# Performance work log

Measured on AMD Instinct MI355X. Metric: run time of the kernel, lower is better.

## Reference

```python
import jax, jax.numpy as jnp
import numpy as np

UNITS = 512
INPUT_SIZE = 512
BATCH = 64
SEQ_LEN = 512


def setup_inputs() -> dict:
    key = jax.random.key(0)
    k_x, k_wx, k_wh = jax.random.split(key, 3)
    scale_x = 1.0 / np.sqrt(INPUT_SIZE)
    scale_h = 1.0 / np.sqrt(UNITS)
    return {
        "x": jax.random.normal(k_x, (BATCH, SEQ_LEN, INPUT_SIZE), dtype=jnp.float32),
        "h0": jnp.zeros((BATCH, UNITS), dtype=jnp.float32),
        "c0": jnp.zeros((BATCH, UNITS), dtype=jnp.float32),
        "Wx": jax.random.normal(k_wx, (INPUT_SIZE, 4 * UNITS), dtype=jnp.float32) * scale_x,
        "Wh": jax.random.normal(k_wh, (UNITS, 4 * UNITS), dtype=jnp.float32) * scale_h,
        "b": jnp.zeros((4 * UNITS,), dtype=jnp.float32),
    }


def reference(x, h0, c0, Wx, Wh, b):
    """LSTM layer over full sequence; returns stacked hidden states [seq_len, batch, units]
    (matching TensorArray.stack() time-major output of the original)."""

    def step(carry, xt):
        h, c = carry
        # fused gate pre-activations: [batch, 4*units]
        z = xt @ Wx + h @ Wh + b
        i, f, g, o = jnp.split(z, 4, axis=-1)  # Keras gate order: i, f, c(g), o
        i = jax.nn.sigmoid(i)
        f = jax.nn.sigmoid(f)
        g = jnp.tanh(g)
        o = jax.nn.sigmoid(o)
        c_new = f * c + i * g
        h_new = o * jnp.tanh(c_new)
        return (h_new, c_new), h_new

    xs = jnp.swapaxes(x, 0, 1)  # [seq_len, batch, input_size]
    (_, _), hs = jax.lax.scan(step, (h0, c0), xs)
    return hs  # [seq_len, batch, units]
```

## Files before the change

kernel.cpp:

```cpp
#include <hip/hip_runtime.h>
#include <stdint.h>


#define OFF_XBF   0ull
#define OFF_HU    33562624ull

typedef short short8 __attribute__((ext_vector_type(8)));
typedef float f32x4 __attribute__((ext_vector_type(4)));
typedef unsigned u32x4 __attribute__((ext_vector_type(4)));

__device__ __forceinline__ unsigned f32_to_bf16(float f) {
    union { float f; unsigned u; } v; v.f = f;
    unsigned u = v.u;
    unsigned r = u + 0x7FFFu + ((u >> 16) & 1u);
    return r >> 16;
}

__global__ void prep_kernel(const float* __restrict__ x,
                            const float* __restrict__ h0,
                            unsigned char* __restrict__ ws) {
    long long i = (long long)blockIdx.x * blockDim.x + threadIdx.x;
    if (i < 2097152) {
        const float4* xs = (const float4*)x + i * 2;
        float4 a = xs[0], b = xs[1];
        unsigned w0 = f32_to_bf16(a.x) | (f32_to_bf16(a.y) << 16);
        unsigned w1 = f32_to_bf16(a.z) | (f32_to_bf16(a.w) << 16);
        unsigned w2 = f32_to_bf16(b.x) | (f32_to_bf16(b.y) << 16);
        unsigned w3 = f32_to_bf16(b.z) | (f32_to_bf16(b.w) << 16);
        uint4 o; o.x = w0; o.y = w1; o.z = w2; o.w = w3;
        ((uint4*)(ws + OFF_XBF))[i] = o;
        return;
    }
    i -= 2097152;
    if (i < 16384) {
        int b = (int)(i >> 8), p = (int)(i & 255);
        unsigned lo = f32_to_bf16(h0[b * 512 + 2 * p]);
        unsigned hi = f32_to_bf16(h0[b * 512 + 2 * p + 1]);
        ((unsigned long long*)(ws + OFF_HU))[(long long)b * 256 + p] =
            (unsigned long long)(lo | (hi << 16)) | (1ull << 32);
    }
}

#define SPIN_LOAD(BASEPTR, TAGV, H0V, H1V)                                     \
    {                                                                          \
        u32x4 p0, p1, p2, p3;                                                  \
        for (;;) {                                                             \
            asm volatile(                                                      \
                "global_load_dwordx4 %0, %4, off sc0 sc1\n\t"                  \
                "global_load_dwordx4 %1, %4, off offset:16 sc0 sc1\n\t"        \
                "global_load_dwordx4 %2, %4, off offset:32 sc0 sc1\n\t"        \
                "global_load_dwordx4 %3, %4, off offset:48 sc0 sc1\n\t"        \
                "s_waitcnt vmcnt(0)"                                           \
                : "=v"(p0), "=v"(p1), "=v"(p2), "=v"(p3)                       \
                : "v"(BASEPTR)                                                 \
                : "memory");                                                   \
            unsigned bad = (p0.y ^ (TAGV)) | (p0.w ^ (TAGV))                   \
                         | (p1.y ^ (TAGV)) | (p1.w ^ (TAGV))                   \
                         | (p2.y ^ (TAGV)) | (p2.w ^ (TAGV))                   \
                         | (p3.y ^ (TAGV)) | (p3.w ^ (TAGV));                  \
            if (!bad) {                                                        \
                H0V.x = p0.x; H0V.y = p0.z; H0V.z = p1.x; H0V.w = p1.z;        \
                H1V.x = p2.x; H1V.y = p2.z; H1V.z = p3.x; H1V.w = p3.z;        \
                break;                                                         \
            }                                                                  \
            __builtin_amdgcn_s_sleep(0);                                       \
        }                                                                      \
    }

__launch_bounds__(256, 1)
__global__ void lstm_kernel(const float* __restrict__ c0,
                            const float* __restrict__ bias,
                            const float* __restrict__ Wx,
                            const float* __restrict__ Wh,
                            float* __restrict__ out,
                            unsigned char* __restrict__ ws) {
    const int tid  = threadIdx.x;
    const int bid  = blockIdx.x;
    const int s    = bid & 7;
    const int jg   = bid >> 3;
    const int lane = tid & 63;
    const int wave = tid >> 6;
    const int nl   = lane & 15;
    const int q    = lane >> 4;
    const int up   = nl & 3;
    const int g    = nl >> 2;

    const unsigned short* xbf = (const unsigned short*)(ws + OFF_XBF);
    unsigned long long* Hu = (unsigned long long*)(ws + OFF_HU);

    __shared__ __align__(16) unsigned char lds[20736];
    float* lds_out = (float*)(lds + 16640);

    const int ncol = g * 512 + jg * 16 + wave * 4 + up;
    short8 fWh[16], fWx[16];
#pragma unroll
    for (int kt = 0; kt < 16; ++kt) {
        const int k0 = kt * 32 + q * 8;
        short8 vh, vx;
#pragma unroll
        for (int j = 0; j < 8; ++j) {
            vh[j] = (short)f32_to_bf16(Wh[(long long)(k0 + j) * 2048 + ncol]);
            vx[j] = (short)f32_to_bf16(Wx[(long long)(k0 + j) * 2048 + ncol]);
        }
        fWh[kt] = vh; fWx[kt] = vx;
    }

    const int ub = jg * 16 + wave * 4 + up;
    const float bi  = bias[ub];
    const float bf_ = bias[512 + ub];
    const float bg  = bias[1024 + ub];
    const float bo  = bias[1536 + ub];

    float cr[4];
#pragma unroll
    for (int r = 0; r < 4; ++r) {
        const int m = q * 4 + r;
        cr[r] = (q < 2) ? c0[(8 * s + m) * 512 + ub] : 0.f;
    }

    const int sm = tid >> 5, sc = tid & 31;
    const int sb = 8 * s + sm;
    const unsigned* xsrc_base = (const unsigned*)xbf + (long long)sb * 131072 + sc * 8;
    unsigned long long* hsrc_base = Hu + sb * 256 + sc * 8;
    uint4* xdst = (uint4*)(lds + sm * 1040 + sc * 32);
    uint4* hdst = (uint4*)(lds + 8320 + sm * 1040 + sc * 32);

    const unsigned char* axp = lds + nl * 1040 + q * 16;
    const unsigned char* ahp = lds + 8320 + nl * 1040 + q * 16;
    const short8 zfrag = {0, 0, 0, 0, 0, 0, 0, 0};

    const int gbase = (lane & 0x30) | (lane & 3);
    const int sl0 = gbase, sl1 = gbase | 4, sl2 = gbase | 8, sl3 = gbase | 12;

    uint4 px0 = *(const uint4*)(xsrc_base);
    uint4 px1 = *(const uint4*)(xsrc_base + 4);
    xdst[0] = px0; xdst[1] = px1;
    px0 = *(const uint4*)(xsrc_base + 256);
    px1 = *(const uint4*)(xsrc_base + 256 + 4);
    __syncthreads();

    f32x4 accx;
    {
        f32x4 a0 = {0.f,0.f,0.f,0.f}, a1 = {0.f,0.f,0.f,0.f};
#pragma unroll
        for (int kt = 0; kt < 16; kt += 2) {
            short8 v0 = (nl < 8) ? *(const short8*)(axp + kt * 64) : zfrag;
            short8 v1 = (nl < 8) ? *(const short8*)(axp + kt * 64 + 64) : zfrag;
            a0 = __builtin_amdgcn_mfma_f32_16x16x32_bf16(v0, fWx[kt], a0, 0, 0, 0);
            a1 = __builtin_amdgcn_mfma_f32_16x16x32_bf16(v1, fWx[kt + 1], a1, 0, 0, 0);
        }
        accx = a0 + a1;
    }
    {
        const unsigned char* hs0 = (const unsigned char*)hsrc_base;
        uint4 h0v, h1v;
        SPIN_LOAD(hs0, 1u, h0v, h1v);
        hdst[0] = h0v; hdst[1] = h1v;
    }
    __syncthreads();

    for (int t = 0; t < 512; ++t) {
        const int wb = (t + 1) & 1;

        f32x4 acch;
        {
            f32x4 a0 = {0.f,0.f,0.f,0.f}, a1 = {0.f,0.f,0.f,0.f};
#pragma unroll
            for (int kt = 0; kt < 16; kt += 2) {
                short8 v0 = (nl < 8) ? *(const short8*)(ahp + kt * 64) : zfrag;
                short8 v1 = (nl < 8) ? *(const short8*)(ahp + kt * 64 + 64) : zfrag;
                a0 = __builtin_amdgcn_mfma_f32_16x16x32_bf16(v0, fWh[kt], a0, 0, 0, 0);
                a1 = __builtin_amdgcn_mfma_f32_16x16x32_bf16(v1, fWh[kt + 1], a1, 0, 0, 0);
            }
            acch = a0 + a1;
        }

        float hn[4]; unsigned hb[4];
#pragma unroll
        for (int r = 0; r < 4; ++r) {
            float zs = accx[r] + acch[r];
            float z0 = __shfl(zs, sl0, 64) + bi;
            float z1 = __shfl(zs, sl1, 64) + bf_;
            float z2 = __shfl(zs, sl2, 64) + bg;
            float z3 = __shfl(zs, sl3, 64) + bo;
            float ig = __fdividef(1.f, 1.f + __expf(-z0));
            float fg = __fdividef(1.f, 1.f + __expf(-z1));
            float z2c = fminf(fmaxf(z2, -20.f), 20.f);
            float e2 = __expf(2.f * z2c);
            float gg = __fdividef(e2 - 1.f, e2 + 1.f);
            float og = __fdividef(1.f, 1.f + __expf(-z3));
            float cn = fg * cr[r] + ig * gg;
            cr[r] = cn;
            float cnc = fminf(fmaxf(cn, -20.f), 20.f);
            float ec = __expf(2.f * cnc);
            hn[r] = og * __fdividef(ec - 1.f, ec + 1.f);
            hb[r] = f32_to_bf16(hn[r]);
        }
        unsigned oth[4];
#pragma unroll
        for (int r = 0; r < 4; ++r)
            oth[r] = (unsigned)__shfl((int)hb[r], lane ^ 1, 64);

        if (q < 2 && g == 0) {
#pragma unroll
            for (int r = 0; r < 4; ++r)
                lds_out[(t & 7) * 128 + (q * 4 + r) * 16 + wave * 4 + up] = hn[r];
            if ((up & 1) == 0) {
#pragma unroll
                for (int r = 0; r < 4; ++r) {
                    unsigned long long v = (unsigned long long)(hb[r] | (oth[r] << 16))
                                         | ((unsigned long long)(unsigned)(t + 2) << 32);
                    __hip_atomic_store(Hu + (size_t)wb * 16384 + (8 * s + q * 4 + r) * 256
                                           + jg * 8 + wave * 2 + (up >> 1),
                                       v, __ATOMIC_RELAXED, __HIP_MEMORY_SCOPE_AGENT);
                }
            }
        }

        xdst[0] = px0; xdst[1] = px1;
        {
            const int tp = (t + 2 < 512) ? (t + 2) : 511;
            px0 = *(const uint4*)(xsrc_base + tp * 256);
            px1 = *(const uint4*)(xsrc_base + tp * 256 + 4);
        }
        __syncthreads();

        if ((t & 7) == 7) {
            const int stp = tid >> 5, brow = (tid >> 2) & 7, qd = tid & 3;
            float4 v = *(const float4*)(lds_out + stp * 128 + brow * 16 + qd * 4);
            *(float4*)(out + (long long)(t - 7 + stp) * 32768
                           + (8 * s + brow) * 512 + jg * 16 + qd * 4) = v;
        }

        {
            f32x4 a0 = {0.f,0.f,0.f,0.f}, a1 = {0.f,0.f,0.f,0.f};
#pragma unroll
            for (int kt = 0; kt < 16; kt += 2) {
                short8 v0 = (nl < 8) ? *(const short8*)(axp + kt * 64) : zfrag;
                short8 v1 = (nl < 8) ? *(const short8*)(axp + kt * 64 + 64) : zfrag;
                a0 = __builtin_amdgcn_mfma_f32_16x16x32_bf16(v0, fWx[kt], a0, 0, 0, 0);
                a1 = __builtin_amdgcn_mfma_f32_16x16x32_bf16(v1, fWx[kt + 1], a1, 0, 0, 0);
            }
            accx = a0 + a1;
        }

        {
            const unsigned char* hs = (const unsigned char*)hsrc_base
                                    + (size_t)wb * 131072;
            const unsigned tag = (unsigned)(t + 2);
            uint4 h0v, h1v;
            SPIN_LOAD(hs, tag, h0v, h1v);
            hdst[0] = h0v; hdst[1] = h1v;
        }
        __syncthreads();
    }
}

extern "C" void kernel_launch(void* const* d_in, const int* in_sizes, int n_in,
                              void* d_out, int out_size, void* d_ws, size_t ws_size,
                              hipStream_t stream) {
    const float* x  = (const float*)d_in[0];
    const float* h0 = (const float*)d_in[1];
    const float* c0 = (const float*)d_in[2];
    const float* Wx = (const float*)d_in[3];
    const float* Wh = (const float*)d_in[4];
    const float* b  = (const float*)d_in[5];
    unsigned char* ws = (unsigned char*)d_ws;
    float* out = (float*)d_out;

    const long long n0 = 2097152 + 16384;
    const int blocks0 = (int)((n0 + 255) / 256);
    hipLaunchKernelGGL(prep_kernel, dim3(blocks0), dim3(256), 0, stream, x, h0, ws);
    hipLaunchKernelGGL(lstm_kernel, dim3(256), dim3(256), 0, stream,
                       c0, b, Wx, Wh, out, ws);
}
```

Measured before the change: 1.746 ms.

## Gate hidden-state spin loads on compact per-group ready flags

```diff
diff --git a/kernel.cpp b/kernel.cpp
--- a/kernel.cpp
+++ b/kernel.cpp
@@ -3,6 +3,7 @@
 
 
 #define OFF_XBF   0ull
+#define OFF_FLAG  33554432ull
 #define OFF_HU    33562624ull
 
 typedef short short8 __attribute__((ext_vector_type(8)));
@@ -38,8 +39,27 @@
         unsigned hi = f32_to_bf16(h0[b * 512 + 2 * p + 1]);
         ((unsigned long long*)(ws + OFF_HU))[(long long)b * 256 + p] =
             (unsigned long long)(lo | (hi << 16)) | (1ull << 32);
+        return;
+    }
+    i -= 16384;
+    if (i < 1024) {
+        ((unsigned*)(ws + OFF_FLAG))[i] = (i < 512) ? 0x00010001u : 0u;
     }
 }
+
+#define FLAG_GATE(FBASE, TAGV)                                                 \
+    {                                                                          \
+        const unsigned expect_ = (TAGV) * 0x10001u;                            \
+        const unsigned* fp_ = (FBASE) + lane;                                  \
+        for (;;) {                                                             \
+            unsigned fv_;                                                      \
+            asm volatile("global_load_dword %0, %1, off sc0 sc1\n\t"           \
+                         "s_waitcnt vmcnt(0)"                                  \
+                         : "=v"(fv_) : "v"(fp_) : "memory");                   \
+            if (!__any((int)(fv_ ^ expect_))) break;                           \
+            __builtin_amdgcn_s_sleep(0);                                       \
+        }                                                                      \
+    }
 
 #define SPIN_LOAD(BASEPTR, TAGV, H0V, H1V)                                     \
     {                                                                          \
@@ -152,6 +172,8 @@
         accx = a0 + a1;
     }
     {
+        const unsigned* fb = (const unsigned*)(ws + OFF_FLAG) + (size_t)s * 64;
+        FLAG_GATE(fb, 1u);
         const unsigned char* hs0 = (const unsigned char*)hsrc_base;
         uint4 h0v, h1v;
         SPIN_LOAD(hs0, 1u, h0v, h1v);
@@ -218,6 +240,16 @@
         }
 
         xdst[0] = px0; xdst[1] = px1;
+
+        asm volatile("s_waitcnt vmcnt(0)" ::: "memory");
+        if (lane == 0) {
+            unsigned short* fp = (unsigned short*)(ws + OFF_FLAG)
+                               + (size_t)(wb * 8 + s) * 128 + jg * 4 + wave;
+            unsigned tv = (unsigned)(t + 2);
+            asm volatile("global_store_short %0, %1, off sc0 sc1"
+                         :: "v"(fp), "v"(tv) : "memory");
+        }
+
         {
             const int tp = (t + 2 < 512) ? (t + 2) : 511;
             px0 = *(const uint4*)(xsrc_base + tp * 256);
@@ -245,9 +277,12 @@
         }
 
         {
+            const unsigned* fb = (const unsigned*)(ws + OFF_FLAG)
+                               + (size_t)(wb * 8 + s) * 64;
+            const unsigned tag = (unsigned)(t + 2);
+            FLAG_GATE(fb, tag);
             const unsigned char* hs = (const unsigned char*)hsrc_base
                                     + (size_t)wb * 131072;
-            const unsigned tag = (unsigned)(t + 2);
             uint4 h0v, h1v;
             SPIN_LOAD(hs, tag, h0v, h1v);
             hdst[0] = h0v; hdst[1] = h1v;
@@ -268,7 +303,7 @@
     unsigned char* ws = (unsigned char*)d_ws;
     float* out = (float*)d_out;
 
-    const long long n0 = 2097152 + 16384;
+    const long long n0 = 2097152 + 16384 + 1024;
     const int blocks0 = (int)((n0 + 255) / 256);
     hipLaunchKernelGGL(prep_kernel, dim3(blocks0), dim3(256), 0, stream, x, h0, ws);
     hipLaunchKernelGGL(lstm_kernel, dim3(256), dim3(256), 0, stream,
```

Result: slower. 2.271 ms (+30.1%).

## Publish hidden state to dual buffers with local and system-scope polling

Applied to the files above, without the earlier changes.

```diff
diff --git a/kernel.cpp b/kernel.cpp
--- a/kernel.cpp
+++ b/kernel.cpp
@@ -3,7 +3,8 @@
 
 
 #define OFF_XBF   0ull
-#define OFF_HU    33562624ull
+#define OFF_HL    33554432ull
+#define OFF_HG    33816576ull
 
 typedef short short8 __attribute__((ext_vector_type(8)));
 typedef float f32x4 __attribute__((ext_vector_type(4)));
@@ -36,33 +37,47 @@
         int b = (int)(i >> 8), p = (int)(i & 255);
         unsigned lo = f32_to_bf16(h0[b * 512 + 2 * p]);
         unsigned hi = f32_to_bf16(h0[b * 512 + 2 * p + 1]);
-        ((unsigned long long*)(ws + OFF_HU))[(long long)b * 256 + p] =
+        unsigned long long v =
             (unsigned long long)(lo | (hi << 16)) | (1ull << 32);
-    }
-}
-
-#define SPIN_LOAD(BASEPTR, TAGV, H0V, H1V)                                     \
+        ((unsigned long long*)(ws + OFF_HL))[(long long)b * 256 + p] = v;
+        ((unsigned long long*)(ws + OFF_HG))[(long long)b * 256 + p] = v;
+    }
+}
+
+#define POLL_ONCE(BASEPTR, CPOL, TAGV, OKV, H0V, H1V)                          \
     {                                                                          \
         u32x4 p0, p1, p2, p3;                                                  \
+        asm volatile(                                                          \
+            "global_load_dwordx4 %0, %4, off " CPOL "\n\t"                     \
+            "global_load_dwordx4 %1, %4, off offset:16 " CPOL "\n\t"           \
+            "global_load_dwordx4 %2, %4, off offset:32 " CPOL "\n\t"           \
+            "global_load_dwordx4 %3, %4, off offset:48 " CPOL "\n\t"           \
+            "s_waitcnt vmcnt(0)"                                               \
+            : "=v"(p0), "=v"(p1), "=v"(p2), "=v"(p3)                           \
+            : "v"(BASEPTR)                                                     \
+            : "memory");                                                       \
+        unsigned bad = (p0.y ^ (TAGV)) | (p0.w ^ (TAGV))                       \
+                     | (p1.y ^ (TAGV)) | (p1.w ^ (TAGV))                       \
+                     | (p2.y ^ (TAGV)) | (p2.w ^ (TAGV))                       \
+                     | (p3.y ^ (TAGV)) | (p3.w ^ (TAGV));                      \
+        OKV = (bad == 0u);                                                     \
+        if (OKV) {                                                             \
+            H0V.x = p0.x; H0V.y = p0.z; H0V.z = p1.x; H0V.w = p1.z;            \
+            H1V.x = p2.x; H1V.y = p2.z; H1V.z = p3.x; H1V.w = p3.z;            \
+        }                                                                      \
+    }
+
+#define SPIN_DUAL(LPTR, GPTR, TAGV, H0V, H1V)                                  \
+    {                                                                          \
+        int ok_ = 0, it_ = 0;                                                  \
         for (;;) {                                                             \
-            asm volatile(                                                      \
-                "global_load_dwordx4 %0, %4, off sc0 sc1\n\t"                  \
-                "global_load_dwordx4 %1, %4, off offset:16 sc0 sc1\n\t"        \
-                "global_load_dwordx4 %2, %4, off offset:32 sc0 sc1\n\t"        \
-                "global_load_dwordx4 %3, %4, off offset:48 sc0 sc1\n\t"        \
-                "s_waitcnt vmcnt(0)"                                           \
-                : "=v"(p0), "=v"(p1), "=v"(p2), "=v"(p3)                       \
-                : "v"(BASEPTR)                                                 \
-                : "memory");                                                   \
-            unsigned bad = (p0.y ^ (TAGV)) | (p0.w ^ (TAGV))                   \
-                         | (p1.y ^ (TAGV)) | (p1.w ^ (TAGV))                   \
-                         | (p2.y ^ (TAGV)) | (p2.w ^ (TAGV))                   \
-                         | (p3.y ^ (TAGV)) | (p3.w ^ (TAGV));                  \
-            if (!bad) {                                                        \
-                H0V.x = p0.x; H0V.y = p0.z; H0V.z = p1.x; H0V.w = p1.z;        \
-                H1V.x = p2.x; H1V.y = p2.z; H1V.z = p3.x; H1V.w = p3.z;        \
-                break;                                                         \
+            POLL_ONCE(LPTR, "sc0", TAGV, ok_, H0V, H1V);                       \
+            if (ok_) break;                                                    \
+            if ((it_ & 7) == 7) {                                              \
+                POLL_ONCE(GPTR, "sc0 sc1", TAGV, ok_, H0V, H1V);               \
+                if (ok_) break;                                                \
             }                                                                  \
+            ++it_;                                                             \
             __builtin_amdgcn_s_sleep(0);                                       \
         }                                                                      \
     }
@@ -86,7 +101,8 @@
     const int g    = nl >> 2;
 
     const unsigned short* xbf = (const unsigned short*)(ws + OFF_XBF);
-    unsigned long long* Hu = (unsigned long long*)(ws + OFF_HU);
+    unsigned long long* HuL = (unsigned long long*)(ws + OFF_HL);
+    unsigned long long* HuG = (unsigned long long*)(ws + OFF_HG);
 
     __shared__ __align__(16) unsigned char lds[20736];
     float* lds_out = (float*)(lds + 16640);
@@ -121,7 +137,8 @@
     const int sm = tid >> 5, sc = tid & 31;
     const int sb = 8 * s + sm;
     const unsigned* xsrc_base = (const unsigned*)xbf + (long long)sb * 131072 + sc * 8;
-    unsigned long long* hsrc_base = Hu + sb * 256 + sc * 8;
+    const unsigned char* hl_base = (const unsigned char*)(HuL + sb * 256 + sc * 8);
+    const unsigned char* hg_base = (const unsigned char*)(HuG + sb * 256 + sc * 8);
     uint4* xdst = (uint4*)(lds + sm * 1040 + sc * 32);
     uint4* hdst = (uint4*)(lds + 8320 + sm * 1040 + sc * 32);
 
@@ -152,9 +169,8 @@
         accx = a0 + a1;
     }
     {
-        const unsigned char* hs0 = (const unsigned char*)hsrc_base;
         uint4 h0v, h1v;
-        SPIN_LOAD(hs0, 1u, h0v, h1v);
+        SPIN_DUAL(hl_base, hg_base, 1u, h0v, h1v);
         hdst[0] = h0v; hdst[1] = h1v;
     }
     __syncthreads();
@@ -210,9 +226,13 @@
                 for (int r = 0; r < 4; ++r) {
                     unsigned long long v = (unsigned long long)(hb[r] | (oth[r] << 16))
                                          | ((unsigned long long)(unsigned)(t + 2) << 32);
-                    __hip_atomic_store(Hu + (size_t)wb * 16384 + (8 * s + q * 4 + r) * 256
-                                           + jg * 8 + wave * 2 + (up >> 1),
-                                       v, __ATOMIC_RELAXED, __HIP_MEMORY_SCOPE_AGENT);
+                    const size_t idx = (size_t)wb * 16384
+                                     + (size_t)(8 * s + q * 4 + r) * 256
+                                     + jg * 8 + wave * 2 + (up >> 1);
+                    asm volatile("global_store_dwordx2 %0, %1, off sc0"
+                                 :: "v"(HuL + idx), "v"(v) : "memory");
+                    asm volatile("global_store_dwordx2 %0, %1, off sc0 sc1"
+                                 :: "v"(HuG + idx), "v"(v) : "memory");
                 }
             }
         }
@@ -245,11 +265,11 @@
         }
 
         {
-            const unsigned char* hs = (const unsigned char*)hsrc_base
-                                    + (size_t)wb * 131072;
+            const unsigned char* hl = hl_base + (size_t)wb * 131072;
+            const unsigned char* hg = hg_base + (size_t)wb * 131072;
             const unsigned tag = (unsigned)(t + 2);
             uint4 h0v, h1v;
-            SPIN_LOAD(hs, tag, h0v, h1v);
+            SPIN_DUAL(hl, hg, tag, h0v, h1v);
             hdst[0] = h0v; hdst[1] = h1v;
         }
         __syncthreads();
```

Result: slower. 2.133 ms (+22.2%).

## Process two batch slices per block, halving grid to 128 blocks

Applied to the files above, without the earlier changes.

```diff
diff --git a/kernel.cpp b/kernel.cpp
--- a/kernel.cpp
+++ b/kernel.cpp
@@ -67,6 +67,73 @@
         }                                                                      \
     }
 
+#define MFMA_LOOP(AP, W, ACC)                                                  \
+    {                                                                          \
+        f32x4 a0_ = {0.f,0.f,0.f,0.f}, a1_ = {0.f,0.f,0.f,0.f};                \
+        _Pragma("unroll")                                                      \
+        for (int kt = 0; kt < 16; kt += 2) {                                   \
+            short8 v0_ = (nl < 8) ? *(const short8*)((AP) + kt * 64) : zfrag;  \
+            short8 v1_ = (nl < 8) ? *(const short8*)((AP) + kt * 64 + 64) : zfrag; \
+            a0_ = __builtin_amdgcn_mfma_f32_16x16x32_bf16(v0_, (W)[kt], a0_, 0, 0, 0); \
+            a1_ = __builtin_amdgcn_mfma_f32_16x16x32_bf16(v1_, (W)[kt + 1], a1_, 0, 0, 0); \
+        }                                                                      \
+        ACC = a0_ + a1_;                                                       \
+    }
+
+#define GATES_PUBLISH(ACCX, ACCH, CR, LDSOUT, SS)                              \
+    {                                                                          \
+        float hn[4]; unsigned hb[4];                                           \
+        _Pragma("unroll")                                                      \
+        for (int r = 0; r < 4; ++r) {                                          \
+            float zs = (ACCX)[r] + (ACCH)[r];                                  \
+            float z0 = __shfl(zs, sl0, 64) + bi;                               \
+            float z1 = __shfl(zs, sl1, 64) + bf_;                              \
+            float z2 = __shfl(zs, sl2, 64) + bg;                               \
+            float z3 = __shfl(zs, sl3, 64) + bo;                               \
+            float ig = __fdividef(1.f, 1.f + __expf(-z0));                     \
+            float fg = __fdividef(1.f, 1.f + __expf(-z1));                     \
+            float z2c = fminf(fmaxf(z2, -20.f), 20.f);                         \
+            float e2 = __expf(2.f * z2c);                                      \
+            float gg = __fdividef(e2 - 1.f, e2 + 1.f);                         \
+            float og = __fdividef(1.f, 1.f + __expf(-z3));                     \
+            float cn = fg * (CR)[r] + ig * gg;                                 \
+            (CR)[r] = cn;                                                      \
+            float cnc = fminf(fmaxf(cn, -20.f), 20.f);                         \
+            float ec = __expf(2.f * cnc);                                      \
+            hn[r] = og * __fdividef(ec - 1.f, ec + 1.f);                       \
+            hb[r] = f32_to_bf16(hn[r]);                                        \
+        }                                                                      \
+        unsigned oth[4];                                                       \
+        _Pragma("unroll")                                                      \
+        for (int r = 0; r < 4; ++r)                                            \
+            oth[r] = (unsigned)__shfl((int)hb[r], lane ^ 1, 64);               \
+        if (q < 2 && g == 0) {                                                 \
+            _Pragma("unroll")                                                  \
+            for (int r = 0; r < 4; ++r)                                        \
+                (LDSOUT)[(t & 7) * 128 + (q * 4 + r) * 16 + wave * 4 + up] = hn[r]; \
+            if ((up & 1) == 0) {                                               \
+                _Pragma("unroll")                                              \
+                for (int r = 0; r < 4; ++r) {                                  \
+                    unsigned long long v = (unsigned long long)(hb[r] | (oth[r] << 16)) \
+                                         | ((unsigned long long)(unsigned)(t + 2) << 32); \
+                    unsigned long long* pp = Hu + (size_t)wb * 16384           \
+                                           + (size_t)(8 * (SS) + q * 4 + r) * 256 \
+                                           + jg * 8 + wave * 2 + (up >> 1);    \
+                    asm volatile("global_store_dwordx2 %0, %1, off sc0 sc1"    \
+                                 :: "v"(pp), "v"(v) : "memory");               \
+                }                                                              \
+            }                                                                  \
+        }                                                                      \
+    }
+
+#define OUT_BURST(LDSOUT, SS)                                                  \
+    {                                                                          \
+        const int stp = tid >> 5, brow = (tid >> 2) & 7, qd = tid & 3;         \
+        float4 v = *(const float4*)((LDSOUT) + stp * 128 + brow * 16 + qd * 4); \
+        *(float4*)(out + (long long)(t - 7 + stp) * 32768                      \
+                       + (8 * (SS) + brow) * 512 + jg * 16 + qd * 4) = v;      \
+    }
+
 __launch_bounds__(256, 1)
 __global__ void lstm_kernel(const float* __restrict__ c0,
                             const float* __restrict__ bias,
@@ -75,9 +142,10 @@
                             float* __restrict__ out,
                             unsigned char* __restrict__ ws) {
     const int tid  = threadIdx.x;
-    const int bid  = blockIdx.x;
-    const int s    = bid & 7;
-    const int jg   = bid >> 3;
+    const int p    = blockIdx.x >> 5;
+    const int jg   = blockIdx.x & 31;
+    const int sA   = p;
+    const int sB   = p + 4;
     const int lane = tid & 63;
     const int wave = tid >> 6;
     const int nl   = lane & 15;
@@ -88,8 +156,9 @@
     const unsigned short* xbf = (const unsigned short*)(ws + OFF_XBF);
     unsigned long long* Hu = (unsigned long long*)(ws + OFF_HU);
 
-    __shared__ __align__(16) unsigned char lds[20736];
-    float* lds_out = (float*)(lds + 16640);
+    __shared__ __align__(16) unsigned char lds[41472];
+    float* lds_outA = (float*)(lds + 33280);
+    float* lds_outB = (float*)(lds + 37376);
 
     const int ncol = g * 512 + jg * 16 + wave * 4 + up;
     short8 fWh[16], fWx[16];
@@ -111,146 +180,108 @@
     const float bg  = bias[1024 + ub];
     const float bo  = bias[1536 + ub];
 
-    float cr[4];
+    float crA[4], crB[4];
 #pragma unroll
     for (int r = 0; r < 4; ++r) {
         const int m = q * 4 + r;
-        cr[r] = (q < 2) ? c0[(8 * s + m) * 512 + ub] : 0.f;
+        crA[r] = (q < 2) ? c0[(8 * sA + m) * 512 + ub] : 0.f;
+        crB[r] = (q < 2) ? c0[(8 * sB + m) * 512 + ub] : 0.f;
     }
 
     const int sm = tid >> 5, sc = tid & 31;
-    const int sb = 8 * s + sm;
-    const unsigned* xsrc_base = (const unsigned*)xbf + (long long)sb * 131072 + sc * 8;
-    unsigned long long* hsrc_base = Hu + sb * 256 + sc * 8;
-    uint4* xdst = (uint4*)(lds + sm * 1040 + sc * 32);
-    uint4* hdst = (uint4*)(lds + 8320 + sm * 1040 + sc * 32);
-
-    const unsigned char* axp = lds + nl * 1040 + q * 16;
-    const unsigned char* ahp = lds + 8320 + nl * 1040 + q * 16;
+    const int sbA = 8 * sA + sm, sbB = 8 * sB + sm;
+    const unsigned* xsrcA = (const unsigned*)xbf + (long long)sbA * 131072 + sc * 8;
+    const unsigned* xsrcB = (const unsigned*)xbf + (long long)sbB * 131072 + sc * 8;
+    unsigned long long* hsrcA = Hu + sbA * 256 + sc * 8;
+    unsigned long long* hsrcB = Hu + sbB * 256 + sc * 8;
+    uint4* xdstA = (uint4*)(lds + sm * 1040 + sc * 32);
+    uint4* xdstB = (uint4*)(lds + 8320 + sm * 1040 + sc * 32);
+    uint4* hdstA = (uint4*)(lds + 16640 + sm * 1040 + sc * 32);
+    uint4* hdstB = (uint4*)(lds + 24960 + sm * 1040 + sc * 32);
+
+    const unsigned char* axpA = lds + nl * 1040 + q * 16;
+    const unsigned char* axpB = lds + 8320 + nl * 1040 + q * 16;
+    const unsigned char* ahpA = lds + 16640 + nl * 1040 + q * 16;
+    const unsigned char* ahpB = lds + 24960 + nl * 1040 + q * 16;
     const short8 zfrag = {0, 0, 0, 0, 0, 0, 0, 0};
 
     const int gbase = (lane & 0x30) | (lane & 3);
     const int sl0 = gbase, sl1 = gbase | 4, sl2 = gbase | 8, sl3 = gbase | 12;
 
-    uint4 px0 = *(const uint4*)(xsrc_base);
-    uint4 px1 = *(const uint4*)(xsrc_base + 4);
-    xdst[0] = px0; xdst[1] = px1;
-    px0 = *(const uint4*)(xsrc_base + 256);
-    px1 = *(const uint4*)(xsrc_base + 256 + 4);
+    uint4 pA0 = *(const uint4*)(xsrcA);
+    uint4 pA1 = *(const uint4*)(xsrcA + 4);
+    uint4 pB0 = *(const uint4*)(xsrcB);
+    uint4 pB1 = *(const uint4*)(xsrcB + 4);
+    xdstA[0] = pA0; xdstA[1] = pA1;
+    xdstB[0] = pB0; xdstB[1] = pB1;
+    pA0 = *(const uint4*)(xsrcA + 256); pA1 = *(const uint4*)(xsrcA + 260);
+    pB0 = *(const uint4*)(xsrcB + 256); pB1 = *(const uint4*)(xsrcB + 260);
     __syncthreads();
 
-    f32x4 accx;
+    f32x4 accxA, accxB;
+    MFMA_LOOP(axpA, fWx, accxA);
+    MFMA_LOOP(axpB, fWx, accxB);
     {
-        f32x4 a0 = {0.f,0.f,0.f,0.f}, a1 = {0.f,0.f,0.f,0.f};
-#pragma unroll
-        for (int kt = 0; kt < 16; kt += 2) {
-            short8 v0 = (nl < 8) ? *(const short8*)(axp + kt * 64) : zfrag;
-            short8 v1 = (nl < 8) ? *(const short8*)(axp + kt * 64 + 64) : zfrag;
-            a0 = __builtin_amdgcn_mfma_f32_16x16x32_bf16(v0, fWx[kt], a0, 0, 0, 0);
-            a1 = __builtin_amdgcn_mfma_f32_16x16x32_bf16(v1, fWx[kt + 1], a1, 0, 0, 0);
-        }
-        accx = a0 + a1;
+        uint4 h0v, h1v;
+        SPIN_LOAD((const unsigned char*)hsrcA, 1u, h0v, h1v);
+        hdstA[0] = h0v; hdstA[1] = h1v;
     }
     {
-        const unsigned char* hs0 = (const unsigned char*)hsrc_base;
         uint4 h0v, h1v;
-        SPIN_LOAD(hs0, 1u, h0v, h1v);
-        hdst[0] = h0v; hdst[1] = h1v;
+        SPIN_LOAD((const unsigned char*)hsrcB, 1u, h0v, h1v);
+        hdstB[0] = h0v; hdstB[1] = h1v;
     }
     __syncthreads();
 
     for (int t = 0; t < 512; ++t) {
         const int wb = (t + 1) & 1;
 
-        f32x4 acch;
-        {
-            f32x4 a0 = {0.f,0.f,0.f,0.f}, a1 = {0.f,0.f,0.f,0.f};
-#pragma unroll
-            for (int kt = 0; kt < 16; kt += 2) {
-                short8 v0 = (nl < 8) ? *(const short8*)(ahp + kt * 64) : zfrag;
-                short8 v1 = (nl < 8) ? *(const short8*)(ahp + kt * 64 + 64) : zfrag;
-                a0 = __builtin_amdgcn_mfma_f32_16x16x32_bf16(v0, fWh[kt], a0, 0, 0, 0);
-                a1 = __builtin_amdgcn_mfma_f32_16x16x32_bf16(v1, fWh[kt + 1], a1, 0, 0, 0);
-            }
-            acch = a0 + a1;
-        }
-
-        float hn[4]; unsigned hb[4];
-#pragma unroll
-        for (int r = 0; r < 4; ++r) {
-            float zs = accx[r] + acch[r];
-            float z0 = __shfl(zs, sl0, 64) + bi;
-            float z1 = __shfl(zs, sl1, 64) + bf_;
-            float z2 = __shfl(zs, sl2, 64) + bg;
-            float z3 = __shfl(zs, sl3, 64) + bo;
-            float ig = __fdividef(1.f, 1.f + __expf(-z0));
-            float fg = __fdividef(1.f, 1.f + __expf(-z1));
-            float z2c = fminf(fmaxf(z2, -20.f), 20.f);
-            float e2 = __expf(2.f * z2c);
-            float gg = __fdividef(e2 - 1.f, e2 + 1.f);
-            float og = __fdividef(1.f, 1.f + __expf(-z3));
-            float cn = fg * cr[r] + ig * gg;
-            cr[r] = cn;
-            float cnc = fminf(fmaxf(cn, -20.f), 20.f);
-            float ec = __expf(2.f * cnc);
-            hn[r] = og * __fdividef(ec - 1.f, ec + 1.f);
-            hb[r] = f32_to_bf16(hn[r]);
-        }
-        unsigned oth[4];
-#pragma unroll
-        for (int r = 0; r < 4; ++r)
-            oth[r] = (unsigned)__shfl((int)hb[r], lane ^ 1, 64);
-
-        if (q < 2 && g == 0) {
-#pragma unroll
-            for (int r = 0; r < 4; ++r)
-                lds_out[(t & 7) * 128 + (q * 4 + r) * 16 + wave * 4 + up] = hn[r];
-            if ((up & 1) == 0) {
-#pragma unroll
-                for (int r = 0; r < 4; ++r) {
-                    unsigned long long v = (unsigned long long)(hb[r] | (oth[r] << 16))
-                                         | ((unsigned long long)(unsigned)(t + 2) << 32);
-                    __hip_atomic_store(Hu + (size_t)wb * 16384 + (8 * s + q * 4 + r) * 256
-                                           + jg * 8 + wave * 2 + (up >> 1),
-                                       v, __ATOMIC_RELAXED, __HIP_MEMORY_SCOPE_AGENT);
-                }
-            }
-        }
-
-        xdst[0] = px0; xdst[1] = px1;
+        {
+            f32x4 acch;
+            MFMA_LOOP(ahpA, fWh, acch);
+            GATES_PUBLISH(accxA, acch, crA, lds_outA, sA);
+        }
+
+        {
+            f32x4 acch;
+            MFMA_LOOP(ahpB, fWh, acch);
+            GATES_PUBLISH(accxB, acch, crB, lds_outB, sB);
+        }
+
+        xdstA[0] = pA0; xdstA[1] = pA1;
+        xdstB[0] = pB0; xdstB[1] = pB1;
         {
             const int tp = (t + 2 < 512) ? (t + 2) : 511;
-            px0 = *(const uint4*)(xsrc_base + tp * 256);
-            px1 = *(const uint4*)(xsrc_base + tp * 256 + 4);
+            pA0 = *(const uint4*)(xsrcA + tp * 256);
+            pA1 = *(const uint4*)(xsrcA + tp * 256 + 4);
+            pB0 = *(const uint4*)(xsrcB + tp * 256);
+            pB1 = *(const uint4*)(xsrcB + tp * 256 + 4);
         }
         __syncthreads();
 
         if ((t & 7) == 7) {
-            const int stp = tid >> 5, brow = (tid >> 2) & 7, qd = tid & 3;
-            float4 v = *(const float4*)(lds_out + stp * 128 + brow * 16 + qd * 4);
-            *(float4*)(out + (long long)(t - 7 + stp) * 32768
-                           + (8 * s + brow) * 512 + jg * 16 + qd * 4) = v;
-        }
-
-        {
-            f32x4 a0 = {0.f,0.f,0.f,0.f}, a1 = {0.f,0.f,0.f,0.f};
-#pragma unroll
-            for (int kt = 0; kt < 16; kt += 2) {
-                short8 v0 = (nl < 8) ? *(const short8*)(axp + kt * 64) : zfrag;
-                short8 v1 = (nl < 8) ? *(const short8*)(axp + kt * 64 + 64) : zfrag;
-                a0 = __builtin_amdgcn_mfma_f32_16x16x32_bf16(v0, fWx[kt], a0, 0, 0, 0);
-                a1 = __builtin_amdgcn_mfma_f32_16x16x32_bf16(v1, fWx[kt + 1], a1, 0, 0, 0);
-            }
-            accx = a0 + a1;
-        }
-
-        {
-            const unsigned char* hs = (const unsigned char*)hsrc_base
+            OUT_BURST(lds_outA, sA);
+            OUT_BURST(lds_outB, sB);
+        }
+
+        MFMA_LOOP(axpA, fWx, accxA);
+        MFMA_LOOP(axpB, fWx, accxB);
+
+        {
+            const unsigned char* hs = (const unsigned char*)hsrcA
                                     + (size_t)wb * 131072;
             const unsigned tag = (unsigned)(t + 2);
             uint4 h0v, h1v;
             SPIN_LOAD(hs, tag, h0v, h1v);
-            hdst[0] = h0v; hdst[1] = h1v;
+            hdstA[0] = h0v; hdstA[1] = h1v;
+        }
+        {
+            const unsigned char* hs = (const unsigned char*)hsrcB
+                                    + (size_t)wb * 131072;
+            const unsigned tag = (unsigned)(t + 2);
+            uint4 h0v, h1v;
+            SPIN_LOAD(hs, tag, h0v, h1v);
+            hdstB[0] = h0v; hdstB[1] = h1v;
         }
         __syncthreads();
     }
@@ -271,6 +302,6 @@
     const long long n0 = 2097152 + 16384;
     const int blocks0 = (int)((n0 + 255) / 256);
     hipLaunchKernelGGL(prep_kernel, dim3(blocks0), dim3(256), 0, stream, x, h0, ws);
-    hipLaunchKernelGGL(lstm_kernel, dim3(256), dim3(256), 0, stream,
+    hipLaunchKernelGGL(lstm_kernel, dim3(128), dim3(256), 0, stream,
                        c0, b, Wx, Wh, out, ws);
 }
```

Result: slower. 3.036 ms (+73.9%).
